# Kernel tuning notes

Hardware: AMD Instinct MI355X
Metric: run time of the kernel (lower is better)

Reference implementation:

```python
import jax, jax.numpy as jnp
import numpy as np

B, T, V, D, H, L = 8, 1024, 8192, 768, 12, 6
DH = D // H
FF = 4 * D
EPS = 1e-5


def setup_inputs() -> dict:
    key = jax.random.key(0)
    ks = jax.random.split(key, 12)
    s = 0.02
    return {
        "idx": jax.random.randint(ks[0], (B, T), 0, V),
        "targets": jax.random.randint(ks[1], (B, T), 0, V),
        "tok_emb": jax.random.normal(ks[2], (V, D), jnp.float32) * s,
        "pos_emb": jax.random.normal(ks[3], (T, D), jnp.float32) * s,
        "ln1_g": jnp.ones((L, D), jnp.float32),
        "ln1_b": jnp.zeros((L, D), jnp.float32),
        "Wq": jax.random.normal(ks[4], (L, H, D, DH), jnp.float32) * s,
        "Wk": jax.random.normal(ks[5], (L, H, D, DH), jnp.float32) * s,
        "Wv": jax.random.normal(ks[6], (L, H, D, DH), jnp.float32) * s,
        "Wproj": jax.random.normal(ks[7], (L, D, D), jnp.float32) * s,
        "bproj": jnp.zeros((L, D), jnp.float32),
        "ln2_g": jnp.ones((L, D), jnp.float32),
        "ln2_b": jnp.zeros((L, D), jnp.float32),
        "W1": jax.random.normal(ks[8], (L, D, FF), jnp.float32) * s,
        "b1": jnp.zeros((L, FF), jnp.float32),
        "W2": jax.random.normal(ks[9], (L, FF, D), jnp.float32) * s,
        "b2": jnp.zeros((L, D), jnp.float32),
        "lnf_g": jnp.ones((D,), jnp.float32),
        "lnf_b": jnp.zeros((D,), jnp.float32),
        "W_lm": jax.random.normal(ks[10], (D, V), jnp.float32) * s,
        "b_lm": jnp.zeros((V,), jnp.float32),
    }


def _ln(x, g, b):
    m = jnp.mean(x, axis=-1, keepdims=True)
    v = jnp.var(x, axis=-1, keepdims=True)
    return (x - m) * jax.lax.rsqrt(v + EPS) * g + b


def reference(idx, targets, tok_emb, pos_emb, ln1_g, ln1_b, Wq, Wk, Wv, Wproj,
              bproj, ln2_g, ln2_b, W1, b1, W2, b2, lnf_g, lnf_b, W_lm, b_lm):
    b, t = idx.shape
    x = tok_emb[idx] + pos_emb[:t]  # [B,T,D]
    mask = jnp.tril(jnp.ones((t, t), bool))
    scale = D ** -0.5  # NOTE: original scales by n_embd**-0.5, not head_size**-0.5

    def step(x, p):
        g1, bb1_, wq, wk, wv, wp, bp, g2, bb2_, w1, bia1, w2, bia2 = p
        h = _ln(x, g1, bb1_)
        q = jnp.einsum('btd,hde->bhte', h, wq)  # [B,H,T,DH]
        k = jnp.einsum('btd,hde->bhte', h, wk)
        v = jnp.einsum('btd,hde->bhte', h, wv)
        scores = jnp.einsum('bhqe,bhke->bhqk', q, k) * scale
        scores = jnp.where(mask, scores, -jnp.inf)
        w = jax.nn.softmax(scores, axis=-1)
        o = jnp.einsum('bhqk,bhke->bhqe', w, v)
        o = o.transpose(0, 2, 1, 3).reshape(b, t, D)  # concat heads
        x = x + o @ wp + bp
        h2 = _ln(x, g2, bb2_)
        x = x + jax.nn.relu(h2 @ w1 + bia1) @ w2 + bia2
        return x, None

    x, _ = jax.lax.scan(step, x, (ln1_g, ln1_b, Wq, Wk, Wv, Wproj, bproj,
                                  ln2_g, ln2_b, W1, b1, W2, b2))
    x = _ln(x, lnf_g, lnf_b)
    logits = x @ W_lm + b_lm  # [B,T,V]
    logp = jax.nn.log_softmax(logits, axis=-1)
    loss = -jnp.take_along_axis(logp, targets[..., None], axis=-1).mean()
    return logits, loss
```

## Files before the change

kernel.cpp:

```cpp
#include <hip/hip_runtime.h>
#include <hip/hip_bf16.h>

typedef unsigned int uint;
typedef unsigned short ushort;

typedef short s16x8 __attribute__((ext_vector_type(8)));
typedef ushort u16x4 __attribute__((ext_vector_type(4)));
typedef float f32x4 __attribute__((ext_vector_type(4)));
typedef uint  u32x4 __attribute__((ext_vector_type(4)));

#define NB 8
#define NT 1024
#define NV 8192
#define ND 768
#define NH 12
#define NL 6
#define NDH 64
#define NFF 3072
#define NTOK (NB*NT)

__device__ __forceinline__ ushort f2bf(float f) {
  uint x = __float_as_uint(f);
  x += 0x7FFFu + ((x >> 16) & 1u);
  return (ushort)(x >> 16);
}
__device__ __forceinline__ float bf2f(ushort u) {
  return __uint_as_float(((uint)u) << 16);
}

__device__ __forceinline__ int swz(int row, int col) {
  return row * 64 + ((((col >> 3) ^ row) & 7) << 3) + (col & 7);
}

__device__ __forceinline__ void gload16(const ushort* g, ushort* l) {
  __builtin_amdgcn_global_load_lds(
      (const __attribute__((address_space(1))) void*)g,
      (__attribute__((address_space(3))) void*)l, 16, 0, 0);
}

__global__ __launch_bounds__(192) void embed_kernel(
    const int* __restrict__ idx, const float* __restrict__ tok,
    const float* __restrict__ pos, ushort* __restrict__ x)
{
  int n = blockIdx.x, t = threadIdx.x;
  int token = idx[n];
  const float4* tp = (const float4*)(tok + (size_t)token * ND);
  const float4* pp = (const float4*)(pos + (size_t)(n & (NT - 1)) * ND);
  float4 a = tp[t], b = pp[t];
  u16x4 r;
  r.x = f2bf(a.x + b.x); r.y = f2bf(a.y + b.y);
  r.z = f2bf(a.z + b.z); r.w = f2bf(a.w + b.w);
  *(u16x4*)&x[(size_t)n * ND + t * 4] = r;
}

__global__ __launch_bounds__(192) void ln_kernel(
    const ushort* __restrict__ x, const float* __restrict__ g,
    const float* __restrict__ b, ushort* __restrict__ out)
{
  int row = blockIdx.x, tid = threadIdx.x;
  const ushort* xr = x + (size_t)row * ND;
  u16x4 xv = *(const u16x4*)&xr[tid * 4];
  float v0 = bf2f(xv.x), v1 = bf2f(xv.y), v2 = bf2f(xv.z), v3 = bf2f(xv.w);
  float s = v0 + v1 + v2 + v3;
  float q = v0 * v0 + v1 * v1 + v2 * v2 + v3 * v3;
  #pragma unroll
  for (int d = 1; d < 64; d <<= 1) { s += __shfl_xor(s, d); q += __shfl_xor(q, d); }
  __shared__ float rs[3], rq[3];
  int w = tid >> 6;
  if ((tid & 63) == 0) { rs[w] = s; rq[w] = q; }
  __syncthreads();
  s = rs[0] + rs[1] + rs[2];
  q = rq[0] + rq[1] + rq[2];
  float mean = s * (1.0f / ND);
  float inv = rsqrtf(q * (1.0f / ND) - mean * mean + 1e-5f);
  float4 gv = *(const float4*)&g[tid * 4];
  float4 bv = *(const float4*)&b[tid * 4];
  u16x4 o;
  o.x = f2bf((v0 - mean) * inv * gv.x + bv.x);
  o.y = f2bf((v1 - mean) * inv * gv.y + bv.y);
  o.z = f2bf((v2 - mean) * inv * gv.z + bv.z);
  o.w = f2bf((v3 - mean) * inv * gv.w + bv.w);
  *(u16x4*)&out[(size_t)row * ND + tid * 4] = o;
}

__global__ __launch_bounds__(256) void transp_tile(
    const float* __restrict__ in, ushort* __restrict__ out,
    int R, int C, int HB, size_t sh, size_t sl)
{
  __shared__ ushort t[64][72];
  const int tid = threadIdx.x;
  int ntx = C >> 6, nty = R >> 6;
  int tpb = ntx * nty;
  int bi = blockIdx.x / tpb;
  int rem = blockIdx.x - bi * tpb;
  int ty = rem / ntx, tx = rem - ty * ntx;
  int r0 = ty << 6, c0 = tx << 6;
  const float* ip = in + (size_t)bi * R * C;
  #pragma unroll
  for (int p = 0; p < 4; ++p) {
    int r = (tid >> 4) + p * 16;
    int c = (tid & 15) * 4;
    float4 v = *(const float4*)&ip[(size_t)(r0 + r) * C + c0 + c];
    t[c + 0][r] = f2bf(v.x); t[c + 1][r] = f2bf(v.y);
    t[c + 2][r] = f2bf(v.z); t[c + 3][r] = f2bf(v.w);
  }
  __syncthreads();
  ushort* op = out + (size_t)(bi / HB) * sl + (size_t)(bi % HB) * sh;
  #pragma unroll
  for (int p = 0; p < 4; ++p) {
    int c = (tid >> 4) + p * 16;
    int r = (tid & 15) * 4;
    u16x4 o = *(const u16x4*)&t[c][r];
    *(u16x4*)&op[(size_t)(c0 + c) * R + r0 + r] = o;
  }
}

template<bool BIAS, bool RELU, bool RESID, int OUT>
__global__ __launch_bounds__(256) void gemm_bt(
    const ushort* __restrict__ A, const ushort* __restrict__ Bt,
    const float* __restrict__ bias, ushort* __restrict__ xres,
    void* __restrict__ outp, ushort* __restrict__ outp2,
    int M, int N, int K)
{
  __shared__ ushort As[8192];
  __shared__ ushort Bs[8192];
  const int tid = threadIdx.x;
  const int lane = tid & 63;
  const int w = tid >> 6;
  const int wr = w >> 1, wc = w & 1;
  const int lg = lane >> 4, li = lane & 15;
  const int m0 = blockIdx.y * 128, n0 = blockIdx.x * 128;

  const int tr = tid >> 3;
  const int tc = ((tid & 7) ^ (tr & 7)) << 3;
  const ushort* gA = &A[(size_t)(m0 + tr) * K + tc];
  const ushort* gB = &Bt[(size_t)(n0 + tr) * K + tc];

  f32x4 acc[4][4];
  #pragma unroll
  for (int i = 0; i < 4; ++i)
    #pragma unroll
    for (int j = 0; j < 4; ++j) { f32x4 z = {0.f,0.f,0.f,0.f}; acc[i][j] = z; }

  for (int kk = 0; kk < K; kk += 64) {
    __syncthreads();
    #pragma unroll
    for (int g = 0; g < 4; ++g) {
      gload16(gA + (size_t)(g * 32) * K + kk, &As[g * 2048 + w * 512]);
      gload16(gB + (size_t)(g * 32) * K + kk, &Bs[g * 2048 + w * 512]);
    }
    __syncthreads();
    #pragma unroll
    for (int kh = 0; kh < 2; ++kh) {
      s16x8 af[4], bfr[4];
      #pragma unroll
      for (int i = 0; i < 4; ++i) {
        int ra = wr * 64 + i * 16 + li;
        int rb = wc * 64 + i * 16 + li;
        int cha = (((kh * 4 + lg) ^ (ra & 7)) << 3);
        int chb = (((kh * 4 + lg) ^ (rb & 7)) << 3);
        af[i]  = *(const s16x8*)&As[ra * 64 + cha];
        bfr[i] = *(const s16x8*)&Bs[rb * 64 + chb];
      }
      #pragma unroll
      for (int i = 0; i < 4; ++i)
        #pragma unroll
        for (int j = 0; j < 4; ++j)
          acc[i][j] = __builtin_amdgcn_mfma_f32_16x16x32_bf16(af[i], bfr[j], acc[i][j], 0, 0, 0);
    }
  }

  const bool isV = (OUT == 3) && (n0 >= 1536);
  #pragma unroll
  for (int i = 0; i < 4; ++i) {
    #pragma unroll
    for (int j = 0; j < 4; ++j) {
      int row0 = m0 + wr * 64 + i * 16 + lg * 4;
      int col  = n0 + wc * 64 + j * 16 + li;
      float bv = BIAS ? bias[col] : 0.f;
      if (isV) {
        int dhg = col - 1536;
        int hh = dhg >> 6, dh = dhg & 63;
        int b_ = row0 >> 10, t0 = row0 & (NT - 1);
        u16x4 o;
        o.x = f2bf(acc[i][j][0]); o.y = f2bf(acc[i][j][1]);
        o.z = f2bf(acc[i][j][2]); o.w = f2bf(acc[i][j][3]);
        *(u16x4*)&outp2[((size_t)(b_ * NH + hh) * 64 + dh) * NT + t0] = o;
      } else {
        #pragma unroll
        for (int ii = 0; ii < 4; ++ii) {
          float val = acc[i][j][ii] + bv;
          if (RELU) val = fmaxf(val, 0.f);
          size_t off = (size_t)(row0 + ii) * N + col;
          if (RESID) { val += bf2f(xres[off]); xres[off] = f2bf(val); }
          if (OUT == 1 || OUT == 3) ((ushort*)outp)[off] = f2bf(val);
          if (OUT == 2) ((float*)outp)[off] = val;
        }
      }
    }
  }
}

__global__ __launch_bounds__(256) void attn_kernel(
    const ushort* __restrict__ qkv, const ushort* __restrict__ vT,
    ushort* __restrict__ o)
{
  __shared__ ushort Ks[64 * 64];
  __shared__ ushort Vt[64 * 64];
  __shared__ ushort Ps[4][32 * 64];

  const int tid = threadIdx.x;
  const int lane = tid & 63;
  const int w = tid >> 6;
  const int lg = lane >> 4;
  const int li = lane & 15;

  int bid = blockIdx.x;
  const int qt = bid & 7;
  const int h = (bid >> 3) % NH;
  const int b = bid / (8 * NH);
  const int q0 = qt * 128 + w * 32;
  const size_t nbase = (size_t)b * NT;
  const int hq = h * NDH;
  const int hk = ND + h * NDH;

  s16x8 aq[2][2];
  #pragma unroll
  for (int f = 0; f < 2; ++f)
    #pragma unroll
    for (int c = 0; c < 2; ++c)
      aq[f][c] = *(const s16x8*)&qkv[(nbase + q0 + f * 16 + li) * (3 * ND) + hq + c * 32 + lg * 8];

  float m_r[2][4], l_r[2][4];
  f32x4 oacc[2][4];
  #pragma unroll
  for (int f = 0; f < 2; ++f)
    #pragma unroll
    for (int i = 0; i < 4; ++i) { m_r[f][i] = -1e30f; l_r[f][i] = 0.f; }
  #pragma unroll
  for (int f = 0; f < 2; ++f)
    #pragma unroll
    for (int n = 0; n < 4; ++n) { f32x4 z = {0.f,0.f,0.f,0.f}; oacc[f][n] = z; }

  const float scale = 0.036084391824351615f;
  const ushort* vTb = vT + (size_t)(b * NH + h) * 64 * NT;

  const int nkc = 2 * qt + 2;
  for (int kc = 0; kc < nkc; ++kc) {
    {
      const int kr = lane >> 3;
      const int ch = lane & 7;
      #pragma unroll
      for (int g = 0; g < 2; ++g) {
        int row = g * 32 + w * 8 + kr;
        gload16(&qkv[(nbase + kc * 64 + row) * (size_t)(3 * ND) + hk + ((ch ^ (row & 7)) << 3)],
                &Ks[(g * 32 + w * 8) * 64]);
        gload16(&vTb[(size_t)row * NT + kc * 64 + ((ch ^ (row & 7)) << 3)],
                &Vt[(g * 32 + w * 8) * 64]);
      }
    }
    __syncthreads();
    if (kc * 64 <= q0 + 31) {
      f32x4 s[2][4];
      #pragma unroll
      for (int kt = 0; kt < 4; ++kt) {
        s16x8 bk[2];
        #pragma unroll
        for (int c = 0; c < 2; ++c)
          bk[c] = *(const s16x8*)&Ks[swz(kt * 16 + li, c * 32 + lg * 8)];
        #pragma unroll
        for (int f = 0; f < 2; ++f) {
          f32x4 z = {0.f,0.f,0.f,0.f}; s[f][kt] = z;
          #pragma unroll
          for (int c = 0; c < 2; ++c)
            s[f][kt] = __builtin_amdgcn_mfma_f32_16x16x32_bf16(aq[f][c], bk[c], s[f][kt], 0, 0, 0);
        }
      }
      #pragma unroll
      for (int f = 0; f < 2; ++f) {
        #pragma unroll
        for (int i = 0; i < 4; ++i) {
          int row = q0 + f * 16 + lg * 4 + i;
          float sv[4]; float mx = -1e30f;
          #pragma unroll
          for (int kt = 0; kt < 4; ++kt) {
            int key = kc * 64 + kt * 16 + li;
            float t = s[f][kt][i] * scale;
            t = (key <= row) ? t : -1e30f;
            sv[kt] = t; mx = fmaxf(mx, t);
          }
          #pragma unroll
          for (int d = 1; d < 16; d <<= 1) mx = fmaxf(mx, __shfl_xor(mx, d));
          float mnew = fmaxf(m_r[f][i], mx);
          float corr = __expf(m_r[f][i] - mnew);
          float ps = 0.f;
          #pragma unroll
          for (int kt = 0; kt < 4; ++kt) {
            float pe = __expf(sv[kt] - mnew);
            ps += pe;
            Ps[w][swz(f * 16 + lg * 4 + i, kt * 16 + li)] = f2bf(pe);
          }
          #pragma unroll
          for (int d = 1; d < 16; d <<= 1) ps += __shfl_xor(ps, d);
          l_r[f][i] = l_r[f][i] * corr + ps;
          m_r[f][i] = mnew;
          #pragma unroll
          for (int n = 0; n < 4; ++n) oacc[f][n][i] *= corr;
        }
      }
      #pragma unroll
      for (int c = 0; c < 2; ++c) {
        s16x8 ap[2], bv[4];
        #pragma unroll
        for (int f = 0; f < 2; ++f)
          ap[f] = *(const s16x8*)&Ps[w][swz(f * 16 + li, c * 32 + lg * 8)];
        #pragma unroll
        for (int n = 0; n < 4; ++n)
          bv[n] = *(const s16x8*)&Vt[swz(n * 16 + li, c * 32 + lg * 8)];
        #pragma unroll
        for (int f = 0; f < 2; ++f)
          #pragma unroll
          for (int n = 0; n < 4; ++n)
            oacc[f][n] = __builtin_amdgcn_mfma_f32_16x16x32_bf16(ap[f], bv[n], oacc[f][n], 0, 0, 0);
      }
    }
    __syncthreads();
  }
  #pragma unroll
  for (int f = 0; f < 2; ++f)
    #pragma unroll
    for (int n = 0; n < 4; ++n)
      #pragma unroll
      for (int i = 0; i < 4; ++i) {
        float val = oacc[f][n][i] / l_r[f][i];
        o[(nbase + q0 + f * 16 + lg * 4 + i) * ND + hq + n * 16 + li] = f2bf(val);
      }
}

__global__ __launch_bounds__(256) void loss_row(
    const float* __restrict__ logits, const int* __restrict__ targets,
    float* __restrict__ rowloss)
{
  int row = blockIdx.x, tid = threadIdx.x;
  const float* lr = logits + (size_t)row * NV;
  const float4* l4 = (const float4*)lr;
  float vals[32];
  float mx = -1e30f;
  #pragma unroll
  for (int p = 0; p < 8; ++p) {
    float4 t = l4[p * 256 + tid];
    vals[p*4+0] = t.x; vals[p*4+1] = t.y; vals[p*4+2] = t.z; vals[p*4+3] = t.w;
    mx = fmaxf(mx, fmaxf(fmaxf(t.x, t.y), fmaxf(t.z, t.w)));
  }
  #pragma unroll
  for (int d = 1; d < 64; d <<= 1) mx = fmaxf(mx, __shfl_xor(mx, d));
  __shared__ float red[4], red2[4];
  int w = tid >> 6, lane = tid & 63;
  if (lane == 0) red[w] = mx;
  __syncthreads();
  mx = fmaxf(fmaxf(red[0], red[1]), fmaxf(red[2], red[3]));
  float sm = 0.f;
  #pragma unroll
  for (int i = 0; i < 32; ++i) sm += __expf(vals[i] - mx);
  #pragma unroll
  for (int d = 1; d < 64; d <<= 1) sm += __shfl_xor(sm, d);
  if (lane == 0) red2[w] = sm;
  __syncthreads();
  if (tid == 0) {
    float total = red2[0] + red2[1] + red2[2] + red2[3];
    float lse = mx + __logf(total);
    rowloss[row] = lse - lr[targets[row]];
  }
}

__global__ __launch_bounds__(256) void loss_reduce(
    const float* __restrict__ rowloss, float* __restrict__ out_loss)
{
  int tid = threadIdx.x;
  float s = 0.f;
  #pragma unroll
  for (int i = 0; i < 32; ++i) s += rowloss[tid + i * 256];
  #pragma unroll
  for (int d = 1; d < 64; d <<= 1) s += __shfl_xor(s, d);
  __shared__ float red[4];
  int w = tid >> 6, lane = tid & 63;
  if (lane == 0) red[w] = s;
  __syncthreads();
  if (tid == 0) {
    float total = red[0] + red[1] + red[2] + red[3];
    out_loss[0] = total * (1.0f / NTOK);
  }
}

extern "C" void kernel_launch(void* const* d_in, const int* in_sizes, int n_in,
                              void* d_out, int out_size, void* d_ws, size_t ws_size,
                              hipStream_t stream)
{
  const int*   idx     = (const int*)d_in[0];
  const int*   targets = (const int*)d_in[1];
  const float* tok     = (const float*)d_in[2];
  const float* pos     = (const float*)d_in[3];
  const float* ln1g    = (const float*)d_in[4];
  const float* ln1b    = (const float*)d_in[5];
  const float* Wq      = (const float*)d_in[6];
  const float* Wk      = (const float*)d_in[7];
  const float* Wv      = (const float*)d_in[8];
  const float* Wp      = (const float*)d_in[9];
  const float* bp      = (const float*)d_in[10];
  const float* ln2g    = (const float*)d_in[11];
  const float* ln2b    = (const float*)d_in[12];
  const float* W1      = (const float*)d_in[13];
  const float* b1      = (const float*)d_in[14];
  const float* W2      = (const float*)d_in[15];
  const float* b2      = (const float*)d_in[16];
  const float* lnfg    = (const float*)d_in[17];
  const float* lnfb    = (const float*)d_in[18];
  const float* Wlm     = (const float*)d_in[19];
  const float* blm     = (const float*)d_in[20];

  char* ob = (char*)d_out;
  ushort* x    = (ushort*)ob;
  ushort* qkvb = (ushort*)(ob + 25165824);
  ushort* mid  = (ushort*)(ob + 25165824);
  ushort* qkvT = (ushort*)(ob + 75497472);
  ushort* wpT  = (ushort*)(ob + 75497472 + 21233664);
  ushort* w1T  = (ushort*)(ob + 75497472 + 28311552);
  ushort* w2T  = (ushort*)(ob + 75497472 + 56623104);
  ushort* vTb  = (ushort*)(ob + 160432128);
  float* logits = (float*)d_out;

  char* ws = (char*)d_ws;
  size_t off = 0;
  auto alloc = [&](size_t bytes) -> void* {
    void* p = ws + off; off += (bytes + 255) & ~(size_t)255; return p;
  };
  ushort* h    = (ushort*)alloc((size_t)NTOK * ND * 2);
  ushort* wlmT = (ushort*)alloc((size_t)ND * NV * 2);
  float*  rowloss = (float*)alloc((size_t)NTOK * 4);

  embed_kernel<<<NTOK, 192, 0, stream>>>(idx, tok, pos, x);

  const size_t LQKV = (size_t)2304 * ND;
  {
    transp_tile<<<NL * NH * 12, 256, 0, stream>>>(Wq, qkvT,                   ND, NDH, NH, (size_t)NDH * ND, LQKV);
    transp_tile<<<NL * NH * 12, 256, 0, stream>>>(Wk, qkvT + (size_t)ND*ND,   ND, NDH, NH, (size_t)NDH * ND, LQKV);
    transp_tile<<<NL * NH * 12, 256, 0, stream>>>(Wv, qkvT + (size_t)2*ND*ND, ND, NDH, NH, (size_t)NDH * ND, LQKV);
    transp_tile<<<NL * 144, 256, 0, stream>>>(Wp, wpT, ND, ND, 1, 0, (size_t)ND * ND);
    transp_tile<<<NL * 576, 256, 0, stream>>>(W1, w1T, ND, NFF, 1, 0, (size_t)ND * NFF);
    transp_tile<<<NL * 576, 256, 0, stream>>>(W2, w2T, NFF, ND, 1, 0, (size_t)ND * NFF);
    transp_tile<<<1536, 256, 0, stream>>>(Wlm, wlmT, ND, NV, 1, 0, (size_t)ND * NV);
  }

  dim3 gqkv(2304 / 128, NTOK / 128);
  dim3 g768(ND / 128, NTOK / 128);
  dim3 gff(NFF / 128, NTOK / 128);
  dim3 glm(NV / 128, NTOK / 128);

  for (int l = 0; l < NL; ++l) {
    ln_kernel<<<NTOK, 192, 0, stream>>>(x, ln1g + l * ND, ln1b + l * ND, h);
    gemm_bt<false,false,false,3><<<gqkv, 256, 0, stream>>>(h, qkvT + l * LQKV, nullptr, nullptr, qkvb, vTb, NTOK, 2304, ND);
    attn_kernel<<<NB * NH * (NT / 128), 256, 0, stream>>>(qkvb, vTb, h);
    gemm_bt<true,false,true,0><<<g768, 256, 0, stream>>>(h, wpT + (size_t)l * ND * ND, bp + l * ND, x, nullptr, nullptr, NTOK, ND, ND);
    ln_kernel<<<NTOK, 192, 0, stream>>>(x, ln2g + l * ND, ln2b + l * ND, h);
    gemm_bt<true,true,false,1><<<gff, 256, 0, stream>>>(h, w1T + (size_t)l * ND * NFF, b1 + (size_t)l * NFF, nullptr, mid, nullptr, NTOK, NFF, ND);
    gemm_bt<true,false,true,0><<<g768, 256, 0, stream>>>(mid, w2T + (size_t)l * ND * NFF, b2 + l * ND, x, nullptr, nullptr, NTOK, ND, NFF);
  }

  ln_kernel<<<NTOK, 192, 0, stream>>>(x, lnfg, lnfb, h);
  gemm_bt<true,false,false,2><<<glm, 256, 0, stream>>>(h, wlmT, blm, nullptr, logits, nullptr, NTOK, NV, ND);

  loss_row<<<NTOK, 256, 0, stream>>>(logits, targets, rowloss);
  loss_reduce<<<1, 256, 0, stream>>>(rowloss, logits + (size_t)NTOK * NV);
}
```

Baseline: 2.225 ms.

## Fuse partial log-sum-exp into LM-head GEMM and merge weight transposes

The LM-head GEMM epilogue now computes, for each row, a per-64-column max and sum-of-exp and writes these partial stats to a workspace buffer. The loss kernel then combines 128 partials per row instead of re-reading the full 8192-wide logits row. This removes a full pass over the 256 MB logits tensor. The seven weight-transpose launches are also merged into one kernel. The GEMM epilogue gains shuffles and exp work, which adds register pressure.

```diff
diff --git a/kernel.cpp b/kernel.cpp
--- a/kernel.cpp
+++ b/kernel.cpp
@@ -83,16 +83,15 @@
   *(u16x4*)&out[(size_t)row * ND + tid * 4] = o;
 }
 
-__global__ __launch_bounds__(256) void transp_tile(
-    const float* __restrict__ in, ushort* __restrict__ out,
-    int R, int C, int HB, size_t sh, size_t sl)
-{
-  __shared__ ushort t[64][72];
+__device__ __forceinline__ void transp_body(
+    ushort (*t)[72], const float* __restrict__ in, ushort* __restrict__ out,
+    int R, int C, int HB, size_t sh, size_t sl, int bid)
+{
   const int tid = threadIdx.x;
   int ntx = C >> 6, nty = R >> 6;
   int tpb = ntx * nty;
-  int bi = blockIdx.x / tpb;
-  int rem = blockIdx.x - bi * tpb;
+  int bi = bid / tpb;
+  int rem = bid - bi * tpb;
   int ty = rem / ntx, tx = rem - ty * ntx;
   int r0 = ty << 6, c0 = tx << 6;
   const float* ip = in + (size_t)bi * R * C;
@@ -115,11 +114,33 @@
   }
 }
 
+__global__ __launch_bounds__(256) void transp_all(
+    const float* __restrict__ Wq, const float* __restrict__ Wk,
+    const float* __restrict__ Wv, const float* __restrict__ Wp,
+    const float* __restrict__ W1, const float* __restrict__ W2,
+    const float* __restrict__ Wlm,
+    ushort* __restrict__ qkvT, ushort* __restrict__ wpT,
+    ushort* __restrict__ w1T, ushort* __restrict__ w2T,
+    ushort* __restrict__ wlmT)
+{
+  __shared__ ushort t[64][72];
+  const size_t LQKV = (size_t)2304 * ND;
+  const size_t SH = (size_t)NDH * ND;
+  int bid = blockIdx.x;
+  if (bid < 864)        transp_body(t, Wq, qkvT,                    ND, NDH, NH, SH, LQKV, bid);
+  else if (bid < 1728)  transp_body(t, Wk, qkvT + (size_t)ND*ND,    ND, NDH, NH, SH, LQKV, bid - 864);
+  else if (bid < 2592)  transp_body(t, Wv, qkvT + (size_t)2*ND*ND,  ND, NDH, NH, SH, LQKV, bid - 1728);
+  else if (bid < 3456)  transp_body(t, Wp, wpT, ND, ND, 1, 0, (size_t)ND * ND, bid - 2592);
+  else if (bid < 6912)  transp_body(t, W1, w1T, ND, NFF, 1, 0, (size_t)ND * NFF, bid - 3456);
+  else if (bid < 10368) transp_body(t, W2, w2T, NFF, ND, 1, 0, (size_t)ND * NFF, bid - 6912);
+  else                  transp_body(t, Wlm, wlmT, ND, NV, 1, 0, (size_t)ND * NV, bid - 10368);
+}
+
 template<bool BIAS, bool RELU, bool RESID, int OUT>
 __global__ __launch_bounds__(256) void gemm_bt(
     const ushort* __restrict__ A, const ushort* __restrict__ Bt,
     const float* __restrict__ bias, ushort* __restrict__ xres,
-    void* __restrict__ outp, ushort* __restrict__ outp2,
+    void* __restrict__ outp, void* __restrict__ outp2,
     int M, int N, int K)
 {
   __shared__ ushort As[8192];
@@ -185,7 +206,7 @@
         u16x4 o;
         o.x = f2bf(acc[i][j][0]); o.y = f2bf(acc[i][j][1]);
         o.z = f2bf(acc[i][j][2]); o.w = f2bf(acc[i][j][3]);
-        *(u16x4*)&outp2[((size_t)(b_ * NH + hh) * 64 + dh) * NT + t0] = o;
+        *(u16x4*)&((ushort*)outp2)[((size_t)(b_ * NH + hh) * 64 + dh) * NT + t0] = o;
       } else {
         #pragma unroll
         for (int ii = 0; ii < 4; ++ii) {
@@ -194,7 +215,32 @@
           size_t off = (size_t)(row0 + ii) * N + col;
           if (RESID) { val += bf2f(xres[off]); xres[off] = f2bf(val); }
           if (OUT == 1 || OUT == 3) ((ushort*)outp)[off] = f2bf(val);
-          if (OUT == 2) ((float*)outp)[off] = val;
+          if (OUT == 2) { ((float*)outp)[off] = val; acc[i][j][ii] = val; }
+        }
+      }
+    }
+  }
+
+  if (OUT == 2) {
+    float2* pstat = (float2*)outp2;
+    #pragma unroll
+    for (int i = 0; i < 4; ++i) {
+      #pragma unroll
+      for (int ii = 0; ii < 4; ++ii) {
+        float mx = acc[i][0][ii];
+        #pragma unroll
+        for (int j = 1; j < 4; ++j) mx = fmaxf(mx, acc[i][j][ii]);
+        #pragma unroll
+        for (int d = 1; d < 16; d <<= 1) mx = fmaxf(mx, __shfl_xor(mx, d));
+        float se = 0.f;
+        #pragma unroll
+        for (int j = 0; j < 4; ++j) se += __expf(acc[i][j][ii] - mx);
+        #pragma unroll
+        for (int d = 1; d < 16; d <<= 1) se += __shfl_xor(se, d);
+        if (li == 0) {
+          int r = m0 + wr * 64 + i * 16 + lg * 4 + ii;
+          float2 v; v.x = mx; v.y = se;
+          pstat[(size_t)r * 128 + (n0 >> 6) + wc] = v;
         }
       }
     }
@@ -337,39 +383,28 @@
       }
 }
 
-__global__ __launch_bounds__(256) void loss_row(
-    const float* __restrict__ logits, const int* __restrict__ targets,
-    float* __restrict__ rowloss)
+__global__ __launch_bounds__(128) void loss_lse(
+    const float2* __restrict__ pstat, const float* __restrict__ logits,
+    const int* __restrict__ targets, float* __restrict__ rowloss)
 {
   int row = blockIdx.x, tid = threadIdx.x;
-  const float* lr = logits + (size_t)row * NV;
-  const float4* l4 = (const float4*)lr;
-  float vals[32];
-  float mx = -1e30f;
-  #pragma unroll
-  for (int p = 0; p < 8; ++p) {
-    float4 t = l4[p * 256 + tid];
-    vals[p*4+0] = t.x; vals[p*4+1] = t.y; vals[p*4+2] = t.z; vals[p*4+3] = t.w;
-    mx = fmaxf(mx, fmaxf(fmaxf(t.x, t.y), fmaxf(t.z, t.w)));
-  }
+  float2 p = pstat[(size_t)row * 128 + tid];
+  float mx = p.x;
   #pragma unroll
   for (int d = 1; d < 64; d <<= 1) mx = fmaxf(mx, __shfl_xor(mx, d));
-  __shared__ float red[4], red2[4];
-  int w = tid >> 6, lane = tid & 63;
-  if (lane == 0) red[w] = mx;
+  __shared__ float sm[2], ss[2];
+  int w = tid >> 6;
+  if ((tid & 63) == 0) sm[w] = mx;
   __syncthreads();
-  mx = fmaxf(fmaxf(red[0], red[1]), fmaxf(red[2], red[3]));
-  float sm = 0.f;
-  #pragma unroll
-  for (int i = 0; i < 32; ++i) sm += __expf(vals[i] - mx);
-  #pragma unroll
-  for (int d = 1; d < 64; d <<= 1) sm += __shfl_xor(sm, d);
-  if (lane == 0) red2[w] = sm;
+  mx = fmaxf(sm[0], sm[1]);
+  float se = p.y * __expf(p.x - mx);
+  #pragma unroll
+  for (int d = 1; d < 64; d <<= 1) se += __shfl_xor(se, d);
+  if ((tid & 63) == 0) ss[w] = se;
   __syncthreads();
   if (tid == 0) {
-    float total = red2[0] + red2[1] + red2[2] + red2[3];
-    float lse = mx + __logf(total);
-    rowloss[row] = lse - lr[targets[row]];
+    float lse = mx + __logf(ss[0] + ss[1]);
+    rowloss[row] = lse - logits[(size_t)row * NV + targets[row]];
   }
 }
 
@@ -437,20 +472,14 @@
   ushort* h    = (ushort*)alloc((size_t)NTOK * ND * 2);
   ushort* wlmT = (ushort*)alloc((size_t)ND * NV * 2);
   float*  rowloss = (float*)alloc((size_t)NTOK * 4);
+  float*  pstat = (float*)alloc((size_t)NTOK * 128 * 8);
 
   embed_kernel<<<NTOK, 192, 0, stream>>>(idx, tok, pos, x);
 
+  transp_all<<<11904, 256, 0, stream>>>(Wq, Wk, Wv, Wp, W1, W2, Wlm,
+                                        qkvT, wpT, w1T, w2T, wlmT);
+
   const size_t LQKV = (size_t)2304 * ND;
-  {
-    transp_tile<<<NL * NH * 12, 256, 0, stream>>>(Wq, qkvT,                   ND, NDH, NH, (size_t)NDH * ND, LQKV);
-    transp_tile<<<NL * NH * 12, 256, 0, stream>>>(Wk, qkvT + (size_t)ND*ND,   ND, NDH, NH, (size_t)NDH * ND, LQKV);
-    transp_tile<<<NL * NH * 12, 256, 0, stream>>>(Wv, qkvT + (size_t)2*ND*ND, ND, NDH, NH, (size_t)NDH * ND, LQKV);
-    transp_tile<<<NL * 144, 256, 0, stream>>>(Wp, wpT, ND, ND, 1, 0, (size_t)ND * ND);
-    transp_tile<<<NL * 576, 256, 0, stream>>>(W1, w1T, ND, NFF, 1, 0, (size_t)ND * NFF);
-    transp_tile<<<NL * 576, 256, 0, stream>>>(W2, w2T, NFF, ND, 1, 0, (size_t)ND * NFF);
-    transp_tile<<<1536, 256, 0, stream>>>(Wlm, wlmT, ND, NV, 1, 0, (size_t)ND * NV);
-  }
-
   dim3 gqkv(2304 / 128, NTOK / 128);
   dim3 g768(ND / 128, NTOK / 128);
   dim3 gff(NFF / 128, NTOK / 128);
@@ -467,8 +496,8 @@
   }
 
   ln_kernel<<<NTOK, 192, 0, stream>>>(x, lnfg, lnfb, h);
-  gemm_bt<true,false,false,2><<<glm, 256, 0, stream>>>(h, wlmT, blm, nullptr, logits, nullptr, NTOK, NV, ND);
-
-  loss_row<<<NTOK, 256, 0, stream>>>(logits, targets, rowloss);
+  gemm_bt<true,false,false,2><<<glm, 256, 0, stream>>>(h, wlmT, blm, nullptr, logits, pstat, NTOK, NV, ND);
+
+  loss_lse<<<NTOK, 128, 0, stream>>>((const float2*)pstat, logits, targets, rowloss);
   loss_reduce<<<1, 256, 0, stream>>>(rowloss, logits + (size_t)NTOK * NV);
 }
```

After: 2.231 ms. No clear change (+0.3%).
